# Performance work log

Measured on AMD Instinct MI355X. Metric: run time of the kernel, lower is better.

## Reference

```python
import jax, jax.numpy as jnp
import numpy as np

B, O, Q, QD, SG = 8, 1024, 2048, 1024, 1200

def setup_inputs() -> dict:
    key = jax.random.key(0)
    k1, k2, k3 = jax.random.split(key, 3)
    query_in = jax.random.normal(k1, (B, O, QD), dtype=jnp.float32)
    context_in = jax.random.normal(k2, (B, Q, SG), dtype=jnp.float32)
    # linear_in.weight initialized uniform(-0.1, 0.1) in the torch module
    W = jax.random.uniform(k3, (SG, QD), dtype=jnp.float32, minval=-0.1, maxval=0.1)
    return {"query_in": query_in, "context_in": context_in, "W": W}

def reference(query_in, context_in, W):
    # general attention: project query from query_dim -> sg_dim (no bias)
    query = jnp.einsum('boq,sq->bos', query_in, W)          # [B, O, SG]
    scores = jnp.einsum('bos,bqs->boq', query, context_in)   # [B, O, Q] (unscaled)
    weights = jax.nn.softmax(scores, axis=-1)                # [B, O, Q]
    mix = jnp.einsum('boq,bqs->bos', weights, context_in)    # [B, O, SG]
    return (mix, weights)
```

## Files before the change

### kernel.cpp

```cpp
#include <hip/hip_runtime.h>
#include <hip/hip_bf16.h>


typedef _Float16 half8 __attribute__((ext_vector_type(8)));
typedef _Float16 half4v __attribute__((ext_vector_type(4)));
typedef float    f32x4 __attribute__((ext_vector_type(4)));

#define AS1C(p) ((const __attribute__((address_space(1))) void*)(p))
#define AS3(p)  ((__attribute__((address_space(3))) void*)(p))

__device__ __forceinline__ void stage_tile(const _Float16* __restrict__ X, _Float16* s,
                                           int t, long row0, long rowmax, int ld, int k0)
{
#pragma unroll
    for (int j = 0; j < 2; ++j) {
        const int L = t + 256 * j;
        const int r = L >> 2;
        const int slot = L & 3;
        const int koff = slot ^ ((r >> 1) & 3);
        long grow = row0 + r; if (grow > rowmax) grow = rowmax;
        const _Float16* src = X + grow * (long)ld + k0 + koff * 8;
        _Float16* dst = s + (long)((t & ~63) + 256 * j) * 8;
        __builtin_amdgcn_global_load_lds(AS1C(src), AS3(dst), 16, 0, 0);
    }
}

__device__ __forceinline__ half8 frag(const _Float16* s, int row, int kslot)
{
    return *(const half8*)(s + row * 32 + ((kslot ^ ((row >> 1) & 3)) << 3));
}

template<bool SPLIT, bool OUT16>
__global__ __launch_bounds__(256) void gemm16(
    const _Float16* __restrict__ Ah, const _Float16* __restrict__ Al,
    const _Float16* __restrict__ Bh, const _Float16* __restrict__ Bl,
    float* __restrict__ Cf, _Float16* __restrict__ Ch, _Float16* __restrict__ Cl,
    int N, int K, int lda, int ldb, int ldc,
    long sA, long sB, long sC)
{
    const int t = threadIdx.x;
    const int bz = blockIdx.z;
    const _Float16* A_h = Ah + bz * sA;
    const _Float16* B_h = Bh + bz * sB;
    const _Float16* A_l = SPLIT ? (Al + bz * sA) : nullptr;
    const _Float16* B_l = SPLIT ? (Bl + bz * sB) : nullptr;

    __shared__ __align__(16) _Float16 sAh[2][128 * 32];
    __shared__ __align__(16) _Float16 sBh[2][128 * 32];
    __shared__ __align__(16) _Float16 sAl[SPLIT ? 2 : 1][SPLIT ? 128 * 32 : 8];
    __shared__ __align__(16) _Float16 sBl[SPLIT ? 2 : 1][SPLIT ? 128 * 32 : 8];

    const long row0 = (long)blockIdx.y * 128;
    const int  col0 = blockIdx.x * 128;

    const int wid = t >> 6, lane = t & 63;
    const int wm = (wid >> 1) * 64, wn = (wid & 1) * 64;
    const int fr = lane & 15, kslot = lane >> 4;

    f32x4 acc[4][4];
#pragma unroll
    for (int i = 0; i < 4; ++i)
#pragma unroll
        for (int j = 0; j < 4; ++j) acc[i][j] = (f32x4){0.f, 0.f, 0.f, 0.f};

    stage_tile(A_h, sAh[0], t, row0, row0 + 127, lda, 0);
    stage_tile(B_h, sBh[0], t, col0, N - 1, ldb, 0);
    if (SPLIT) {
        stage_tile(A_l, sAl[0], t, row0, row0 + 127, lda, 0);
        stage_tile(B_l, sBl[0], t, col0, N - 1, ldb, 0);
    }
    __syncthreads();

    int cur = 0;
    for (int k0 = 0; k0 < K; k0 += 32) {
        if (k0 + 32 < K) {
            const int nxt = cur ^ 1, kn = k0 + 32;
            stage_tile(A_h, sAh[nxt], t, row0, row0 + 127, lda, kn);
            stage_tile(B_h, sBh[nxt], t, col0, N - 1, ldb, kn);
            if (SPLIT) {
                stage_tile(A_l, sAl[nxt], t, row0, row0 + 127, lda, kn);
                stage_tile(B_l, sBl[nxt], t, col0, N - 1, ldb, kn);
            }
        }

        half8 a_h[4], b_h[4], a_l[4], b_l[4];
#pragma unroll
        for (int i = 0; i < 4; ++i) {
            a_h[i] = frag(sAh[cur], wm + i * 16 + fr, kslot);
            b_h[i] = frag(sBh[cur], wn + i * 16 + fr, kslot);
            if (SPLIT) {
                a_l[i] = frag(sAl[cur], wm + i * 16 + fr, kslot);
                b_l[i] = frag(sBl[cur], wn + i * 16 + fr, kslot);
            }
        }
#pragma unroll
        for (int mi = 0; mi < 4; ++mi)
#pragma unroll
            for (int ni = 0; ni < 4; ++ni) {
                acc[mi][ni] = __builtin_amdgcn_mfma_f32_16x16x32_f16(a_h[mi], b_h[ni], acc[mi][ni], 0, 0, 0);
                if (SPLIT) {
                    acc[mi][ni] = __builtin_amdgcn_mfma_f32_16x16x32_f16(a_h[mi], b_l[ni], acc[mi][ni], 0, 0, 0);
                    acc[mi][ni] = __builtin_amdgcn_mfma_f32_16x16x32_f16(a_l[mi], b_h[ni], acc[mi][ni], 0, 0, 0);
                }
            }

        __syncthreads();
        cur ^= 1;
    }

    const int r4 = (lane >> 4) * 4;
    float* C_f = OUT16 ? nullptr : (Cf + bz * sC);
#pragma unroll
    for (int mi = 0; mi < 4; ++mi)
#pragma unroll
        for (int ni = 0; ni < 4; ++ni) {
            const int colg = col0 + wn + ni * 16 + fr;
#pragma unroll
            for (int r = 0; r < 4; ++r) {
                const long rowg = row0 + wm + mi * 16 + r4 + r;
                const float v = acc[mi][ni][r];
                if (OUT16) {
                    if (colg < ldc) {
                        const float vv = (colg < N) ? v : 0.f;
                        const _Float16 hi = (_Float16)vv;
                        const _Float16 lo = (_Float16)(vv - (float)hi);
                        Ch[rowg * ldc + colg] = hi;
                        Cl[rowg * ldc + colg] = lo;
                    }
                } else {
                    if (colg < N) C_f[rowg * (long)ldc + colg] = v;
                }
            }
        }
}

__global__ __launch_bounds__(256) void qw_cvt(
    const float* __restrict__ Q, _Float16* __restrict__ QH, _Float16* __restrict__ QL,
    const float* __restrict__ Wt, _Float16* __restrict__ WH, _Float16* __restrict__ WL)
{
    const long NQ = 8192L * 1024 / 4;
    const long NT = NQ + 1200L * 1024 / 4;
    for (long i = (long)blockIdx.x * 256 + threadIdx.x; i < NT; i += (long)gridDim.x * 256) {
        const float* src; _Float16 *dh, *dl; long j;
        if (i < NQ) { j = i; src = Q; dh = QH; dl = QL; }
        else        { j = i - NQ; src = Wt; dh = WH; dl = WL; }
        float4 v = *(const float4*)(src + j * 4);
        const _Float16 h0 = (_Float16)v.x, h1 = (_Float16)v.y, h2 = (_Float16)v.z, h3 = (_Float16)v.w;
        const _Float16 l0 = (_Float16)(v.x - (float)h0), l1 = (_Float16)(v.y - (float)h1);
        const _Float16 l2 = (_Float16)(v.z - (float)h2), l3 = (_Float16)(v.w - (float)h3);
        *(half4v*)(dh + j * 4) = (half4v){h0, h1, h2, h3};
        *(half4v*)(dl + j * 4) = (half4v){l0, l1, l2, l3};
    }
}

__global__ __launch_bounds__(256) void ctx_prep(const float* __restrict__ X,
    _Float16* __restrict__ H, _Float16* __restrict__ L, _Float16* __restrict__ T)
{
    const int b = blockIdx.z;
    const float* Xb = X + (long)b * 2048 * 1200;
    _Float16* Hb = H + (long)b * 2048 * 1216;
    _Float16* Lb = L + (long)b * 2048 * 1216;
    _Float16* Tb = T + (long)b * 1200 * 2048;
    __shared__ _Float16 tl[32][33];
    const int tx = threadIdx.x & 31, ty = threadIdx.x >> 5;
    const int s0 = blockIdx.x * 32, q0 = blockIdx.y * 32;
#pragma unroll
    for (int p = 0; p < 4; ++p) {
        const int q = q0 + ty + p * 8, s = s0 + tx;
        const float v = (s < 1200) ? Xb[(long)q * 1200 + s] : 0.f;
        const _Float16 hi = (_Float16)v;
        Hb[(long)q * 1216 + s] = hi;
        Lb[(long)q * 1216 + s] = (_Float16)(v - (float)hi);
        tl[tx][ty + p * 8] = hi;
    }
    __syncthreads();
#pragma unroll
    for (int p = 0; p < 4; ++p) {
        const int s = s0 + ty + p * 8;
        if (s < 1200) Tb[(long)s * 2048 + q0 + tx] = tl[ty + p * 8][tx];
    }
}

__global__ __launch_bounds__(256) void softmax_k(float* __restrict__ w, _Float16* __restrict__ w16)
{
    float* p = w + (long)blockIdx.x * 2048;
    half4v* p16 = (half4v*)(w16 + (long)blockIdx.x * 2048);
    const int t = threadIdx.x;
    float4 v0 = ((const float4*)p)[t];
    float4 v1 = ((const float4*)p)[t + 256];

    float m = fmaxf(fmaxf(fmaxf(v0.x, v0.y), fmaxf(v0.z, v0.w)),
                    fmaxf(fmaxf(v1.x, v1.y), fmaxf(v1.z, v1.w)));
#pragma unroll
    for (int off = 1; off < 64; off <<= 1) m = fmaxf(m, __shfl_xor(m, off));
    __shared__ float redm[4], reds[4];
    const int wave = t >> 6, lane = t & 63;
    if (lane == 0) redm[wave] = m;
    __syncthreads();
    m = fmaxf(fmaxf(redm[0], redm[1]), fmaxf(redm[2], redm[3]));

    float e[8];
    e[0] = __expf(v0.x - m); e[1] = __expf(v0.y - m);
    e[2] = __expf(v0.z - m); e[3] = __expf(v0.w - m);
    e[4] = __expf(v1.x - m); e[5] = __expf(v1.y - m);
    e[6] = __expf(v1.z - m); e[7] = __expf(v1.w - m);

    float s = ((e[0] + e[1]) + (e[2] + e[3])) + ((e[4] + e[5]) + (e[6] + e[7]));
#pragma unroll
    for (int off = 1; off < 64; off <<= 1) s += __shfl_xor(s, off);
    if (lane == 0) reds[wave] = s;
    __syncthreads();
    s = (reds[0] + reds[1]) + (reds[2] + reds[3]);

    const float inv = 1.0f / s;
    float o0 = e[0] * inv, o1 = e[1] * inv, o2 = e[2] * inv, o3 = e[3] * inv;
    float o4 = e[4] * inv, o5 = e[5] * inv, o6 = e[6] * inv, o7 = e[7] * inv;
    ((float4*)p)[t]       = make_float4(o0, o1, o2, o3);
    ((float4*)p)[t + 256] = make_float4(o4, o5, o6, o7);
    p16[t]       = (half4v){(_Float16)o0, (_Float16)o1, (_Float16)o2, (_Float16)o3};
    p16[t + 256] = (half4v){(_Float16)o4, (_Float16)o5, (_Float16)o6, (_Float16)o7};
}

extern "C" void kernel_launch(void* const* d_in, const int* in_sizes, int n_in,
                              void* d_out, int out_size, void* d_ws, size_t ws_size,
                              hipStream_t stream)
{
    const float* query_in = (const float*)d_in[0];
    const float* context  = (const float*)d_in[1];
    const float* W        = (const float*)d_in[2];

    float* mix    = (float*)d_out;
    float* scores = (float*)d_out + 9830400LL;

    _Float16* qh  = (_Float16*)d_ws;
    _Float16* ql  = qh  + 8388608;
    _Float16* wh  = ql  + 8388608;
    _Float16* wl  = wh  + 1228800;
    _Float16* ch  = wl  + 1228800;
    _Float16* cl  = ch  + 19922944;
    _Float16* ct  = cl  + 19922944;
    _Float16* qeh = ct  + 19660800;
    _Float16* qel = qeh + 9961472;
    _Float16* w16 = qel + 9961472;

    dim3 blk(256);

    qw_cvt<<<2400, blk, 0, stream>>>(query_in, qh, ql, W, wh, wl);
    ctx_prep<<<dim3(38, 64, 8), blk, 0, stream>>>(context, ch, cl, ct);

    gemm16<true, true><<<dim3(10, 64, 1), blk, 0, stream>>>(
        qh, ql, wh, wl, nullptr, qeh, qel,
        1200, 1024, 1024, 1024, 1216, 0, 0, 0);

    gemm16<true, false><<<dim3(16, 8, 8), blk, 0, stream>>>(
        qeh, qel, ch, cl, scores, nullptr, nullptr,
        2048, 1216, 1216, 1216, 2048, 1024L * 1216, 2048L * 1216, 1024L * 2048);

    softmax_k<<<dim3(8192), blk, 0, stream>>>(scores, w16);

    gemm16<false, false><<<dim3(10, 8, 8), blk, 0, stream>>>(
        w16, nullptr, ct, nullptr, mix, nullptr, nullptr,
        1200, 2048, 2048, 2048, 1200, 1024L * 2048, 1200L * 2048, 1024L * 1200);
}
```

Baseline: 532.8 us.

## Add 256x256-tile 8-wave pipelined split-fp16 kernel for the scores GEMM

Replaces the generic 128-tile gemm16 for the query·context scores GEMM with a dedicated 512-thread kernel using 256x256 output tiles. It stages hi and lo fp16 halves into a four-slot LDS ring with direct global-to-LDS loads, waits on explicit vmcnt counts, and raises wave priority around the MFMA bursts. The aim is more data reuse per tile and loads overlapped with compute. In exchange the kernel needs 128 KB of LDS and many accumulator registers, and launches only 256 blocks, which may underfill the GPU.

```diff
diff --git a/kernel.cpp b/kernel.cpp
--- a/kernel.cpp
+++ b/kernel.cpp
@@ -8,6 +8,12 @@
 
 #define AS1C(p) ((const __attribute__((address_space(1))) void*)(p))
 #define AS3(p)  ((__attribute__((address_space(3))) void*)(p))
+
+#define WAITV8() do { asm volatile("s_waitcnt vmcnt(8)" ::: "memory"); __builtin_amdgcn_sched_barrier(0); } while(0)
+#define WAITV4() do { asm volatile("s_waitcnt vmcnt(4)" ::: "memory"); __builtin_amdgcn_sched_barrier(0); } while(0)
+#define WAITV0() do { asm volatile("s_waitcnt vmcnt(0)" ::: "memory"); __builtin_amdgcn_sched_barrier(0); } while(0)
+#define WAITL0() do { asm volatile("s_waitcnt lgkmcnt(0)" ::: "memory"); __builtin_amdgcn_sched_barrier(0); } while(0)
+
 
 __device__ __forceinline__ void stage_tile(const _Float16* __restrict__ X, _Float16* s,
                                            int t, long row0, long rowmax, int ld, int k0)
@@ -25,9 +31,128 @@
     }
 }
 
+__device__ __forceinline__ void stage256(const _Float16* __restrict__ X, _Float16* s,
+                                         int t, long row0, int ld, int k0)
+{
+#pragma unroll
+    for (int j = 0; j < 2; ++j) {
+        const int L = t + 512 * j;
+        const int r = L >> 2;
+        const int slot = L & 3;
+        const int koff = slot ^ ((r >> 1) & 3);
+        const _Float16* src = X + (row0 + r) * (long)ld + k0 + koff * 8;
+        _Float16* dst = s + (long)((t & ~63) + 512 * j) * 8;
+        __builtin_amdgcn_global_load_lds(AS1C(src), AS3(dst), 16, 0, 0);
+    }
+}
+
 __device__ __forceinline__ half8 frag(const _Float16* s, int row, int kslot)
 {
     return *(const half8*)(s + row * 32 + ((kslot ^ ((row >> 1) & 3)) << 3));
+}
+
+#define T2K 38
+__global__ __launch_bounds__(512, 2) void gemm2_8p(
+    const _Float16* __restrict__ Ahp, const _Float16* __restrict__ Alp,
+    const _Float16* __restrict__ Bhp, const _Float16* __restrict__ Blp,
+    float* __restrict__ Cf)
+{
+    const int t = threadIdx.x;
+    const int bz = blockIdx.z;
+    const _Float16* A_h = Ahp + bz * (1024L * 1216);
+    const _Float16* A_l = Alp + bz * (1024L * 1216);
+    const _Float16* B_h = Bhp + bz * (2048L * 1216);
+    const _Float16* B_l = Blp + bz * (2048L * 1216);
+
+    __shared__ __align__(16) _Float16 slots[4][2][256 * 32];
+
+    const long row0 = (long)blockIdx.y * 256;
+    const long col0 = (long)blockIdx.x * 256;
+
+    const int wid = t >> 6, lane = t & 63;
+    const int wr = wid >> 2, wc = wid & 3;
+    const int fr = lane & 15, kslot = lane >> 4;
+
+    f32x4 acc[8][4];
+#pragma unroll
+    for (int i = 0; i < 8; ++i)
+#pragma unroll
+        for (int j = 0; j < 4; ++j) acc[i][j] = (f32x4){0.f, 0.f, 0.f, 0.f};
+
+    stage256(A_h, &slots[0][0][0], t, row0, 1216, 0);
+    stage256(B_h, &slots[0][1][0], t, col0, 1216, 0);
+    stage256(A_l, &slots[1][0][0], t, row0, 1216, 0);
+    stage256(B_l, &slots[1][1][0], t, col0, 1216, 0);
+    stage256(A_h, &slots[2][0][0], t, row0, 1216, 32);
+    stage256(B_h, &slots[2][1][0], t, col0, 1216, 32);
+
+    for (int tt = 0; tt < T2K; ++tt) {
+        const int s0 = (2 * tt) & 3, s1 = (2 * tt + 1) & 3;
+
+        if (tt < T2K - 1) WAITV8(); else WAITV4();
+        __builtin_amdgcn_s_barrier();
+
+        half8 a_h[8], b_h[4];
+#pragma unroll
+        for (int i = 0; i < 8; ++i) a_h[i] = frag(&slots[s0][0][0], wr * 128 + i * 16 + fr, kslot);
+#pragma unroll
+        for (int i = 0; i < 4; ++i) b_h[i] = frag(&slots[s0][1][0], wc * 64 + i * 16 + fr, kslot);
+
+        if (tt < T2K - 1) {
+            const int k0 = (tt + 1) * 32, sl = (2 * tt + 3) & 3;
+            stage256(A_l, &slots[sl][0][0], t, row0, 1216, k0);
+            stage256(B_l, &slots[sl][1][0], t, col0, 1216, k0);
+        }
+        __builtin_amdgcn_s_barrier();
+        WAITL0();
+        __builtin_amdgcn_s_setprio(1);
+#pragma unroll
+        for (int mi = 0; mi < 8; ++mi)
+#pragma unroll
+            for (int ni = 0; ni < 4; ++ni)
+                acc[mi][ni] = __builtin_amdgcn_mfma_f32_16x16x32_f16(a_h[mi], b_h[ni], acc[mi][ni], 0, 0, 0);
+        __builtin_amdgcn_s_setprio(0);
+
+        if (tt < T2K - 1) WAITV8(); else WAITV0();
+        __builtin_amdgcn_s_barrier();
+
+        half8 a_l[8], b_l[4];
+#pragma unroll
+        for (int i = 0; i < 8; ++i) a_l[i] = frag(&slots[s1][0][0], wr * 128 + i * 16 + fr, kslot);
+#pragma unroll
+        for (int i = 0; i < 4; ++i) b_l[i] = frag(&slots[s1][1][0], wc * 64 + i * 16 + fr, kslot);
+
+        if (tt < T2K - 2) {
+            const int k0 = (tt + 2) * 32, sl = (2 * tt + 4) & 3;
+            stage256(A_h, &slots[sl][0][0], t, row0, 1216, k0);
+            stage256(B_h, &slots[sl][1][0], t, col0, 1216, k0);
+        }
+        __builtin_amdgcn_s_barrier();
+        WAITL0();
+        __builtin_amdgcn_s_setprio(1);
+#pragma unroll
+        for (int mi = 0; mi < 8; ++mi)
+#pragma unroll
+            for (int ni = 0; ni < 4; ++ni) {
+                acc[mi][ni] = __builtin_amdgcn_mfma_f32_16x16x32_f16(a_h[mi], b_l[ni], acc[mi][ni], 0, 0, 0);
+                acc[mi][ni] = __builtin_amdgcn_mfma_f32_16x16x32_f16(a_l[mi], b_h[ni], acc[mi][ni], 0, 0, 0);
+            }
+        __builtin_amdgcn_s_setprio(0);
+    }
+
+    const int r4 = (lane >> 4) * 4;
+    float* C = Cf + bz * (1024L * 2048);
+#pragma unroll
+    for (int mi = 0; mi < 8; ++mi)
+#pragma unroll
+        for (int ni = 0; ni < 4; ++ni) {
+            const long colg = col0 + wc * 64 + ni * 16 + fr;
+#pragma unroll
+            for (int r = 0; r < 4; ++r) {
+                const long rowg = row0 + wr * 128 + mi * 16 + r4 + r;
+                C[rowg * 2048 + colg] = acc[mi][ni][r];
+            }
+        }
 }
 
 template<bool SPLIT, bool OUT16>
@@ -252,9 +377,7 @@
         qh, ql, wh, wl, nullptr, qeh, qel,
         1200, 1024, 1024, 1024, 1216, 0, 0, 0);
 
-    gemm16<true, false><<<dim3(16, 8, 8), blk, 0, stream>>>(
-        qeh, qel, ch, cl, scores, nullptr, nullptr,
-        2048, 1216, 1216, 1216, 2048, 1024L * 1216, 2048L * 1216, 1024L * 2048);
+    gemm2_8p<<<dim3(8, 4, 8), dim3(512), 0, stream>>>(qeh, qel, ch, cl, scores);
 
     softmax_k<<<dim3(8192), blk, 0, stream>>>(scores, w16);
 
```

New measurement: 521.3 us. 2.2% less time.
